# Optimization experiments

Hardware: AMD Instinct MI355X
Metric: run time of the kernel (lower is better)

Reference implementation:

```python
import jax, jax.numpy as jnp
import numpy as np

N_CLASSES = 4
N_FEATURES = 13
N_HIDDEN = 13
N_STEPS = 100
FORGET_BIAS = 1.0


def setup_inputs() -> dict:
    key = jax.random.key(0)
    ks = jax.random.split(key, 10)
    B = 32768
    return {
        "x_input": jax.random.normal(ks[0], (B, N_STEPS, N_FEATURES), dtype=jnp.float32),
        # input projection (tf.random.normal mean=0.5 in original; values irrelevant for correctness test)
        "w_hidden": jax.random.normal(ks[1], (N_FEATURES, N_HIDDEN), dtype=jnp.float32) * 0.5 + 0.5,
        "b_hidden": jax.random.normal(ks[2], (N_HIDDEN,), dtype=jnp.float32) * 0.5 + 0.5,
        # BasicLSTMCell params: kernel [input_dim + hidden, 4*hidden], gate order (i, j, f, o)
        "lstm0_kernel": jax.random.normal(ks[3], (N_HIDDEN + N_HIDDEN, 4 * N_HIDDEN), dtype=jnp.float32) * 0.2,
        "lstm0_bias": jnp.zeros((4 * N_HIDDEN,), dtype=jnp.float32),
        "lstm1_kernel": jax.random.normal(ks[4], (N_HIDDEN + N_HIDDEN, 4 * N_HIDDEN), dtype=jnp.float32) * 0.2,
        "lstm1_bias": jnp.zeros((4 * N_HIDDEN,), dtype=jnp.float32),
        "w_output": jax.random.normal(ks[5], (N_HIDDEN, N_CLASSES), dtype=jnp.float32) * 0.5 + 0.5,
        "b_output": jax.random.normal(ks[6], (N_CLASSES,), dtype=jnp.float32) * 0.5 + 0.5,
    }


def _lstm_cell(x, c, h, kernel, bias):
    # BasicLSTMCell: z = [x; h] @ W + b, split -> i, j, f, o
    z = jnp.concatenate([x, h], axis=-1) @ kernel + bias
    i, j, f, o = jnp.split(z, 4, axis=-1)
    c_new = c * jax.nn.sigmoid(f + FORGET_BIAS) + jax.nn.sigmoid(i) * jnp.tanh(j)
    h_new = jnp.tanh(c_new) * jax.nn.sigmoid(o)
    return c_new, h_new


def reference(x_input, w_hidden, b_hidden, lstm0_kernel, lstm0_bias,
              lstm1_kernel, lstm1_bias, w_output, b_output):
    B = x_input.shape[0]
    # input projection + relu, batched over all timesteps: [B,T,F] -> [T,B,H]
    hidden = jax.nn.relu(jnp.einsum('btf,fh->bth', x_input, w_hidden) + b_hidden)
    hidden = jnp.transpose(hidden, (1, 0, 2))  # [T, B, H]

    zeros = jnp.zeros((B, N_HIDDEN), dtype=x_input.dtype)
    init = (zeros, zeros, zeros, zeros)  # (c0, h0, c1, h1)

    def step(carry, x_t):
        c0, h0, c1, h1 = carry
        c0, h0 = _lstm_cell(x_t, c0, h0, lstm0_kernel, lstm0_bias)
        c1, h1 = _lstm_cell(h0, c1, h1, lstm1_kernel, lstm1_bias)
        return (c0, h0, c1, h1), None

    (c0, h0, c1, h1), _ = jax.lax.scan(step, init, hidden)
    # last output of top LSTM layer -> output projection
    return h1 @ w_output + b_output
```

## Files before the change

### kernel.cpp

```cpp
#include <hip/hip_runtime.h>
#include <cstdint>

typedef __bf16          bf16x8 __attribute__((ext_vector_type(8)));
typedef float           f32x4  __attribute__((ext_vector_type(4)));
typedef unsigned short  u16x8  __attribute__((ext_vector_type(8)));
typedef unsigned int    u32x4  __attribute__((ext_vector_type(4)));

#define MFMA16(a,b,c) __builtin_amdgcn_mfma_f32_16x16x32_bf16((a),(b),(c),0,0,0)

__device__ __forceinline__ float rcpf(float x) { return __builtin_amdgcn_rcpf(x); }
__device__ __forceinline__ float ex2(float x)  { return __builtin_amdgcn_exp2f(x); }

__device__ __forceinline__ void split2(float v, unsigned short& hi, unsigned short& lo) {
    unsigned u = __builtin_bit_cast(unsigned, v);
    hi = (unsigned short)(u >> 16);
    float rem = v - __builtin_bit_cast(float, u & 0xffff0000u);
    lo = (unsigned short)(__builtin_bit_cast(unsigned, rem) >> 16);
}
__device__ __forceinline__ __bf16 bfbits(unsigned short b) { return __builtin_bit_cast(__bf16, b); }

__device__ __forceinline__ unsigned packhi2(float a, float b) {
    return __builtin_amdgcn_perm(__builtin_bit_cast(unsigned, b),
                                 __builtin_bit_cast(unsigned, a), 0x07060302u);
}
__device__ __forceinline__ float truncrem(float v) {
    return v - __builtin_bit_cast(float, __builtin_bit_cast(unsigned, v) & 0xffff0000u);
}


constexpr float SN1 = -1.4426950408889634f;
constexpr float SN2 = -2.8853900817779268f;
constexpr float C2  =  2.8853900817779268f;

__global__ __launch_bounds__(128, 4)
void lstm_fused(const float* __restrict__ x,
                const float* __restrict__ w_hidden,
                const float* __restrict__ b_hidden,
                const float* __restrict__ k0,
                const float* __restrict__ b0,
                const float* __restrict__ k1,
                const float* __restrict__ b1,
                const float* __restrict__ w_out,
                const float* __restrict__ b_out,
                float* __restrict__ out)
{
    __shared__ __attribute__((aligned(16))) unsigned short xh_s[2][2][384];
    __shared__ __attribute__((aligned(16))) unsigned short h0_s[2][2][384];
    __shared__ __attribute__((aligned(16))) unsigned short h1_s[2][384];
    __shared__ __attribute__((aligned(16))) float          zp_s[2][256];

    const int lane = threadIdx.x & 63;
    const int role = threadIdx.x >> 6;
    const int col  = lane & 15;
    const int q    = lane >> 4;
    const int qh   = q & 1;
    const int s0   = blockIdx.x * 16;

    {
        unsigned short* a0 = &xh_s[0][0][0];
        unsigned short* a1 = &h0_s[0][0][0];
        for (int idx = threadIdx.x; idx < 1536; idx += 128) {
            unsigned short v = ((idx % 24) == 13 && ((idx / 384) & 1) == 0)
                             ? (unsigned short)0x3F80 : (unsigned short)0;
            a0[idx] = v; a1[idx] = v;
        }
        unsigned short* a2 = &h1_s[0][0];
        for (int idx = threadIdx.x; idx < 768; idx += 128) {
            unsigned short v = ((idx % 24) == 13 && ((idx / 384) & 1) == 0)
                             ? (unsigned short)0x3F80 : (unsigned short)0;
            a2[idx] = v;
        }
    }

    const float* kp = role ? k1 : k0;
    const float* bb = role ? b1 : b0;
    bf16x8 Kh[4], Kl[4];
    #pragma unroll
    for (int g = 0; g < 4; ++g) {
        const float sg = (g == 1) ? SN2 : SN1;
        bf16x8 hv{}, lv{};
        #pragma unroll
        for (int j = 0; j < 8; ++j) {
            int k = 8 * q + j;
            float w = 0.f;
            if (col < 13) {
                if (k < 13)                 w = kp[k * 52 + 13 * g + col];
                else if (k == 13)           w = bb[13 * g + col] + (g == 2 ? 1.f : 0.f);
                else if (k >= 16 && k < 29) w = kp[(13 + k - 16) * 52 + 13 * g + col];
            }
            w *= sg;
            unsigned short h_, l_;
            split2(w, h_, l_);
            hv[j] = bfbits(h_); lv[j] = bfbits(l_);
        }
        Kh[g] = hv; Kl[g] = lv;
    }

    bf16x8 Ph{}, Pl{};
    if (role) {
        #pragma unroll
        for (int j = 0; j < 8; ++j) {
            int k = 8 * q + j;
            float w = 0.f;
            if (col < 13) {
                if (k < 13)       w = w_hidden[k * 13 + col];
                else if (k == 13) w = b_hidden[col];
            }
            unsigned short h_, l_;
            split2(w, h_, l_);
            Ph[j] = bfbits(h_); Pl[j] = bfbits(l_);
        }
    }

    const float* xrow = x + (size_t)(s0 + col) * 1300;

    auto elem = [&](float zi, float zj, float zf, float zo, float& cs) -> float {
        float a   = ex2(zi);
        float b   = ex2(zj);
        float fe  = ex2(zf);
        float g   = ex2(zo);
        float opa = 1.f + a, opb = 1.f + b, opf = 1.f + fe;
        float pab = opa * opb;
        float r1  = rcpf(pab * opf);
        float tt  = fmaf(b, C2, -C2);
        float cn  = fmaf(cs, pab, tt * opf) * r1;
        cs = cn;
        float d   = ex2(cn);
        float r2  = rcpf((1.f + d) * (1.f + g));
        return (1.f - d) * r2;
    };

    auto cell = [&](const unsigned short* inH, const unsigned short* hidH,
                    unsigned short* outH, float* cst) {
        const unsigned short* pA = (q < 2) ? inH : hidH;
        bf16x8 ah = __builtin_bit_cast(bf16x8, *(const u16x8*)(pA + col * 24 + 8 * qh));
        bf16x8 al = __builtin_bit_cast(bf16x8, *(const u16x8*)(pA + 384 + col * 24 + 8 * qh));
        f32x4 z0 = {0.f,0.f,0.f,0.f}, z1 = z0, z2 = z0, z3 = z0;
        z0 = MFMA16(ah, Kh[0], z0); z0 = MFMA16(al, Kh[0], z0); z0 = MFMA16(ah, Kl[0], z0);
        z1 = MFMA16(ah, Kh[1], z1); z1 = MFMA16(al, Kh[1], z1); z1 = MFMA16(ah, Kl[1], z1);
        z2 = MFMA16(ah, Kh[2], z2); z2 = MFMA16(al, Kh[2], z2); z2 = MFMA16(ah, Kl[2], z2);
        z3 = MFMA16(ah, Kh[3], z3); z3 = MFMA16(al, Kh[3], z3); z3 = MFMA16(ah, Kl[3], z3);
        #pragma unroll
        for (int r = 0; r < 4; ++r) {
            float hv = elem(z0[r], z1[r], z2[r], z3[r], cst[r]);
            unsigned short hh, hl;
            split2(hv, hh, hl);
            if (col < 13) {
                outH[(4 * q + r) * 24 + col]       = hh;
                outH[384 + (4 * q + r) * 24 + col] = hl;
            }
        }
    };

    auto loadx = [&](int t, float* xv) {
        if (q < 2) {
            const float* p = xrow + t * 13 + 8 * q;
            const int lim = q ? 4 : 7;
            #pragma unroll
            for (int j = 0; j < 8; ++j) {
                int off = j > lim ? lim : j;
                xv[j] = p[off];
            }
        }
    };

    auto projmfma = [&](const float* xv, float* zpo) {
        bf16x8 axh{}, axl{};
        if (q < 2) {
            unsigned hw0 = packhi2(xv[0], xv[1]);
            unsigned hw1 = packhi2(xv[2], xv[3]);
            unsigned hw2 = packhi2(xv[4], xv[5]);
            unsigned hw3 = packhi2(xv[6], xv[7]);
            unsigned lw0 = packhi2(truncrem(xv[0]), truncrem(xv[1]));
            unsigned lw1 = packhi2(truncrem(xv[2]), truncrem(xv[3]));
            unsigned lw2 = packhi2(truncrem(xv[4]), truncrem(xv[5]));
            unsigned lw3 = packhi2(truncrem(xv[6]), truncrem(xv[7]));
            if (q == 1) {
                hw2 = (hw2 & 0xffffu) | 0x3F800000u;
                lw2 &= 0xffffu;
                hw3 = 0u; lw3 = 0u;
            }
            u32x4 hv = {hw0, hw1, hw2, hw3};
            u32x4 lv = {lw0, lw1, lw2, lw3};
            axh = __builtin_bit_cast(bf16x8, hv);
            axl = __builtin_bit_cast(bf16x8, lv);
        }
        f32x4 zp = {0.f,0.f,0.f,0.f};
        zp = MFMA16(axh, Ph, zp);
        zp = MFMA16(axl, Ph, zp);
        zp = MFMA16(axh, Pl, zp);
        *(f32x4*)(zpo + lane * 4) = zp;
    };

    auto finish = [&](const float* zpi, unsigned short* oH) {
        f32x4 zp = *(const f32x4*)(zpi + lane * 4);
        #pragma unroll
        for (int r = 0; r < 4; ++r) {
            float v = fmaxf(zp[r], 0.f);
            unsigned short hh, hl;
            split2(v, hh, hl);
            if (col < 13) {
                oH[(4 * q + r) * 24 + col]       = hh;
                oH[384 + (4 * q + r) * 24 + col] = hl;
            }
        }
    };

    float cst[4] = {0.f, 0.f, 0.f, 0.f};
    float xA[8], xB[8];

    if (role) loadx(0, xA);
    __syncthreads();
    if (role) { projmfma(xA, &zp_s[0][0]); loadx(1, xB); }
    __syncthreads();

    for (int i = 0; i < 100; i += 2) {
        if (role == 0) {
            finish(&zp_s[0][0], &xh_s[0][0][0]);
            cell(&xh_s[0][0][0], &h0_s[1][0][0], &h0_s[0][0][0], cst);
        } else {
            if (i > 0) cell(&h0_s[1][0][0], &h1_s[0][0], &h1_s[0][0], cst);
            if (i < 98) loadx(i + 2, xA);
            projmfma(xB, &zp_s[1][0]);
        }
        __syncthreads();
        if (role == 0) {
            finish(&zp_s[1][0], &xh_s[1][0][0]);
            cell(&xh_s[1][0][0], &h0_s[0][0][0], &h0_s[1][0][0], cst);
        } else {
            cell(&h0_s[0][0][0], &h1_s[0][0], &h1_s[0][0], cst);
            if (i < 97) loadx(i + 3, xB);
            if (i < 98) projmfma(xA, &zp_s[0][0]);
        }
        __syncthreads();
    }

    if (role) {
        cell(&h0_s[1][0][0], &h1_s[0][0], &h1_s[0][0], cst);

        bf16x8 Oh{}, Ol{};
        #pragma unroll
        for (int j = 0; j < 8; ++j) {
            int k = 8 * q + j;
            float w = 0.f;
            if (col < 4) {
                if (k < 13)       w = w_out[k * 4 + col];
                else if (k == 13) w = b_out[col];
            }
            unsigned short h_, l_;
            split2(w, h_, l_);
            Oh[j] = bfbits(h_); Ol[j] = bfbits(l_);
        }
        const unsigned short* pA = &h1_s[0][0];
        bf16x8 ah = __builtin_bit_cast(bf16x8, *(const u16x8*)(pA + col * 24 + 8 * qh));
        bf16x8 al = __builtin_bit_cast(bf16x8, *(const u16x8*)(pA + 384 + col * 24 + 8 * qh));
        f32x4 zf = {0.f,0.f,0.f,0.f};
        zf = MFMA16(ah, Oh, zf);
        zf = MFMA16(al, Oh, zf);
        zf = MFMA16(ah, Ol, zf);
        if (col < 4) {
            #pragma unroll
            for (int r = 0; r < 4; ++r)
                out[(size_t)(s0 + 4 * q + r) * 4 + col] = zf[r];
        }
    }
}

extern "C" void kernel_launch(void* const* d_in, const int* in_sizes, int n_in,
                              void* d_out, int out_size, void* d_ws, size_t ws_size,
                              hipStream_t stream) {
    (void)in_sizes; (void)n_in; (void)d_ws; (void)ws_size; (void)out_size;
    lstm_fused<<<dim3(2048), dim3(128), 0, stream>>>(
        (const float*)d_in[0], (const float*)d_in[1], (const float*)d_in[2],
        (const float*)d_in[3], (const float*)d_in[4], (const float*)d_in[5],
        (const float*)d_in[6], (const float*)d_in[7], (const float*)d_in[8],
        (float*)d_out);
}
```

Measured before the change: 355.7 us.

## Merge two-wavefront layer pipeline into a single wavefront per block

```diff
diff --git a/kernel.cpp b/kernel.cpp
--- a/kernel.cpp
+++ b/kernel.cpp
@@ -32,7 +32,7 @@
 constexpr float SN2 = -2.8853900817779268f;
 constexpr float C2  =  2.8853900817779268f;
 
-__global__ __launch_bounds__(128, 4)
+__global__ __launch_bounds__(64, 2)
 void lstm_fused(const float* __restrict__ x,
                 const float* __restrict__ w_hidden,
                 const float* __restrict__ b_hidden,
@@ -47,10 +47,8 @@
     __shared__ __attribute__((aligned(16))) unsigned short xh_s[2][2][384];
     __shared__ __attribute__((aligned(16))) unsigned short h0_s[2][2][384];
     __shared__ __attribute__((aligned(16))) unsigned short h1_s[2][384];
-    __shared__ __attribute__((aligned(16))) float          zp_s[2][256];
 
     const int lane = threadIdx.x & 63;
-    const int role = threadIdx.x >> 6;
     const int col  = lane & 15;
     const int q    = lane >> 4;
     const int qh   = q & 1;
@@ -59,45 +57,49 @@
     {
         unsigned short* a0 = &xh_s[0][0][0];
         unsigned short* a1 = &h0_s[0][0][0];
-        for (int idx = threadIdx.x; idx < 1536; idx += 128) {
+        for (int idx = lane; idx < 1536; idx += 64) {
             unsigned short v = ((idx % 24) == 13 && ((idx / 384) & 1) == 0)
                              ? (unsigned short)0x3F80 : (unsigned short)0;
             a0[idx] = v; a1[idx] = v;
         }
         unsigned short* a2 = &h1_s[0][0];
-        for (int idx = threadIdx.x; idx < 768; idx += 128) {
+        for (int idx = lane; idx < 768; idx += 64) {
             unsigned short v = ((idx % 24) == 13 && ((idx / 384) & 1) == 0)
                              ? (unsigned short)0x3F80 : (unsigned short)0;
             a2[idx] = v;
         }
     }
 
-    const float* kp = role ? k1 : k0;
-    const float* bb = role ? b1 : b0;
-    bf16x8 Kh[4], Kl[4];
+    bf16x8 K0h[4], K0l[4], K1h[4], K1l[4];
     #pragma unroll
-    for (int g = 0; g < 4; ++g) {
-        const float sg = (g == 1) ? SN2 : SN1;
-        bf16x8 hv{}, lv{};
-        #pragma unroll
-        for (int j = 0; j < 8; ++j) {
-            int k = 8 * q + j;
-            float w = 0.f;
-            if (col < 13) {
-                if (k < 13)                 w = kp[k * 52 + 13 * g + col];
-                else if (k == 13)           w = bb[13 * g + col] + (g == 2 ? 1.f : 0.f);
-                else if (k >= 16 && k < 29) w = kp[(13 + k - 16) * 52 + 13 * g + col];
-            }
-            w *= sg;
-            unsigned short h_, l_;
-            split2(w, h_, l_);
-            hv[j] = bfbits(h_); lv[j] = bfbits(l_);
-        }
-        Kh[g] = hv; Kl[g] = lv;
+    for (int L = 0; L < 2; ++L) {
+        const float* kp = L ? k1 : k0;
+        const float* bb = L ? b1 : b0;
+        #pragma unroll
+        for (int g = 0; g < 4; ++g) {
+            const float sg = (g == 1) ? SN2 : SN1;
+            bf16x8 hv{}, lv{};
+            #pragma unroll
+            for (int j = 0; j < 8; ++j) {
+                int k = 8 * q + j;
+                float w = 0.f;
+                if (col < 13) {
+                    if (k < 13)                 w = kp[k * 52 + 13 * g + col];
+                    else if (k == 13)           w = bb[13 * g + col] + (g == 2 ? 1.f : 0.f);
+                    else if (k >= 16 && k < 29) w = kp[(13 + k - 16) * 52 + 13 * g + col];
+                }
+                w *= sg;
+                unsigned short h_, l_;
+                split2(w, h_, l_);
+                hv[j] = bfbits(h_); lv[j] = bfbits(l_);
+            }
+            if (L) { K1h[g] = hv; K1l[g] = lv; }
+            else   { K0h[g] = hv; K0l[g] = lv; }
+        }
     }
 
     bf16x8 Ph{}, Pl{};
-    if (role) {
+    {
         #pragma unroll
         for (int j = 0; j < 8; ++j) {
             int k = 8 * q + j;
@@ -131,7 +133,8 @@
     };
 
     auto cell = [&](const unsigned short* inH, const unsigned short* hidH,
-                    unsigned short* outH, float* cst) {
+                    unsigned short* outH, float* cst,
+                    const bf16x8 (&Kh)[4], const bf16x8 (&Kl)[4]) {
         const unsigned short* pA = (q < 2) ? inH : hidH;
         bf16x8 ah = __builtin_bit_cast(bf16x8, *(const u16x8*)(pA + col * 24 + 8 * qh));
         bf16x8 al = __builtin_bit_cast(bf16x8, *(const u16x8*)(pA + 384 + col * 24 + 8 * qh));
@@ -164,7 +167,7 @@
         }
     };
 
-    auto projmfma = [&](const float* xv, float* zpo) {
+    auto projfull = [&](const float* xv, unsigned short* oH) {
         bf16x8 axh{}, axl{};
         if (q < 2) {
             unsigned hw0 = packhi2(xv[0], xv[1]);
@@ -189,11 +192,6 @@
         zp = MFMA16(axh, Ph, zp);
         zp = MFMA16(axl, Ph, zp);
         zp = MFMA16(axh, Pl, zp);
-        *(f32x4*)(zpo + lane * 4) = zp;
-    };
-
-    auto finish = [&](const float* zpi, unsigned short* oH) {
-        f32x4 zp = *(const f32x4*)(zpi + lane * 4);
         #pragma unroll
         for (int r = 0; r < 4; ++r) {
             float v = fmaxf(zp[r], 0.f);
@@ -206,38 +204,31 @@
         }
     };
 
-    float cst[4] = {0.f, 0.f, 0.f, 0.f};
+    float cst0[4] = {0.f, 0.f, 0.f, 0.f};
+    float cst1[4] = {0.f, 0.f, 0.f, 0.f};
     float xA[8], xB[8];
 
-    if (role) loadx(0, xA);
+    loadx(0, xA);
     __syncthreads();
-    if (role) { projmfma(xA, &zp_s[0][0]); loadx(1, xB); }
-    __syncthreads();
+    projfull(xA, &xh_s[0][0][0]);
+    loadx(1, xB);
 
     for (int i = 0; i < 100; i += 2) {
-        if (role == 0) {
-            finish(&zp_s[0][0], &xh_s[0][0][0]);
-            cell(&xh_s[0][0][0], &h0_s[1][0][0], &h0_s[0][0][0], cst);
-        } else {
-            if (i > 0) cell(&h0_s[1][0][0], &h1_s[0][0], &h1_s[0][0], cst);
-            if (i < 98) loadx(i + 2, xA);
-            projmfma(xB, &zp_s[1][0]);
-        }
-        __syncthreads();
-        if (role == 0) {
-            finish(&zp_s[1][0], &xh_s[1][0][0]);
-            cell(&xh_s[1][0][0], &h0_s[0][0][0], &h0_s[1][0][0], cst);
-        } else {
-            cell(&h0_s[0][0][0], &h1_s[0][0], &h1_s[0][0], cst);
-            if (i < 97) loadx(i + 3, xB);
-            if (i < 98) projmfma(xA, &zp_s[0][0]);
-        }
-        __syncthreads();
-    }
-
-    if (role) {
-        cell(&h0_s[1][0][0], &h1_s[0][0], &h1_s[0][0], cst);
-
+        if (i < 98) loadx(i + 2, xA);
+        projfull(xB, &xh_s[1][0][0]);
+        cell(&xh_s[0][0][0], &h0_s[1][0][0], &h0_s[0][0][0], cst0, K0h, K0l);
+        if (i > 0)
+            cell(&h0_s[1][0][0], &h1_s[0][0], &h1_s[0][0], cst1, K1h, K1l);
+
+        if (i < 97) loadx(i + 3, xB);
+        if (i < 98) projfull(xA, &xh_s[0][0][0]);
+        cell(&xh_s[1][0][0], &h0_s[0][0][0], &h0_s[1][0][0], cst0, K0h, K0l);
+        cell(&h0_s[0][0][0], &h1_s[0][0], &h1_s[0][0], cst1, K1h, K1l);
+    }
+
+    cell(&h0_s[1][0][0], &h1_s[0][0], &h1_s[0][0], cst1, K1h, K1l);
+
+    {
         bf16x8 Oh{}, Ol{};
         #pragma unroll
         for (int j = 0; j < 8; ++j) {
@@ -270,7 +261,7 @@
                               void* d_out, int out_size, void* d_ws, size_t ws_size,
                               hipStream_t stream) {
     (void)in_sizes; (void)n_in; (void)d_ws; (void)ws_size; (void)out_size;
-    lstm_fused<<<dim3(2048), dim3(128), 0, stream>>>(
+    lstm_fused<<<dim3(2048), dim3(64), 0, stream>>>(
         (const float*)d_in[0], (const float*)d_in[1], (const float*)d_in[2],
         (const float*)d_in[3], (const float*)d_in[4], (const float*)d_in[5],
         (const float*)d_in[6], (const float*)d_in[7], (const float*)d_in[8],
```

Result: slower. 386.6 us (+8.7%).
